# Kernel tuning notes

Hardware: AMD Instinct MI355X
Metric: run time of the kernel (lower is better)

The kernel has to match this reference:

```python
import jax, jax.numpy as jnp
import numpy as np

MARGIN = 0.2
ALPHA = 2.0
BETA = 1.5
ANGLE_THRESHOLD = 30.0
EPS_PD = 1e-6   # F.pairwise_distance eps
EPS_CS = 1e-8   # F.cosine_similarity eps
NEG_INF = -1e30
POS_INF = 1e30


def setup_inputs() -> dict:
    key = jax.random.key(0)
    k1, k2, k3 = jax.random.split(key, 3)
    B, F, A = 4096, 512, 3
    features = jax.random.normal(k1, (B, F), dtype=jnp.float32)
    labels = jax.random.randint(k2, (B,), 0, 256)
    angles = jax.random.uniform(k3, (B, A), dtype=jnp.float32) * 90.0  # degrees
    features_orig = jax.random.normal(jax.random.fold_in(key, 7), (B, F), dtype=jnp.float32)
    return {"features": features, "labels": labels, "angles": angles, "features_orig": features_orig}


def _cosine_sim_matrix(f):
    norms = jnp.linalg.norm(f, axis=1)
    denom = jnp.maximum(norms[:, None] * norms[None, :], EPS_CS)
    return (f @ f.T) / denom


def _forward(features, labels, angles, features_orig):
    B = features.shape[0]
    idx = jnp.arange(B)
    # pairwise angle distances [B,B] (torch.cdist p=2)
    adist = jnp.sqrt(jnp.sum((angles[:, None, :] - angles[None, :, :]) ** 2, axis=-1))
    same = labels[:, None] == labels[None, :]
    same = same & ~jnp.eye(B, dtype=bool)          # exclude self
    diff = labels[:, None] != labels[None, :]
    has_pos = same.any(axis=1)
    has_neg = diff.any(axis=1)
    valid = has_pos & has_neg
    # hardest positive: same label, largest angle difference
    pos_idx = jnp.argmax(jnp.where(same, adist, NEG_INF), axis=1)
    # hardest negative: among diff-label within angle threshold, most similar feature;
    # else diff-label with smallest angle difference
    sim = _cosine_sim_matrix(features)
    similar = diff & (adist < ANGLE_THRESHOLD)
    sim_any = similar.any(axis=1)
    neg_idx_hard = jnp.argmax(jnp.where(similar, sim, NEG_INF), axis=1)
    neg_idx_far = jnp.argmin(jnp.where(diff, adist, POS_INF), axis=1)
    neg_idx = jnp.where(sim_any, neg_idx_hard, neg_idx_far)
    # triplet distances (F.pairwise_distance adds eps to the diff)
    a = features
    p = features[pos_idx]
    n = features[neg_idx]
    pos_d = jnp.linalg.norm(a - p + EPS_PD, axis=1)
    neg_d = jnp.linalg.norm(a - n + EPS_PD, axis=1)
    # angle-based weights (non-differentiable, matches .item() in torch)
    pa = adist[idx, pos_idx]
    na = adist[idx, neg_idx]
    w = jnp.where(pa > 45.0, ALPHA, 1.0) * jnp.where(na < 15.0, BETA, 1.0)
    basic = jax.nn.relu(pos_d - neg_d + MARGIN)
    vmask = valid.astype(features.dtype)
    cnt = jnp.maximum(vmask.sum(), 1.0)
    triplet_loss = jnp.sum(w * basic * vmask) / cnt
    # reconstruction term
    num = jnp.sum(features * features_orig, axis=1)
    den = jnp.maximum(jnp.linalg.norm(features, axis=1) * jnp.linalg.norm(features_orig, axis=1), EPS_CS)
    recon = 1.0 - jnp.mean(num / den)
    return triplet_loss + 0.1 * recon


def reference(features, labels, angles, features_orig):
    return _forward(features, labels, angles, features_orig)
```

## Files before the change

### kernel.cpp

```cpp
#include <hip/hip_runtime.h>
#include <math.h>

#define BN 4096
#define FD 512
#define TT 128
#define BK 64
#define NJT (BN / TT)
#define NPAIR (NJT * (NJT + 1) / 2)
#define NBLK NPAIR
#define NPC 128
#define NJR 32
#define JR (BN / NJR)
#define NABLK (NJR * (BN / 256))

typedef __attribute__((ext_vector_type(8))) __bf16 bf16x8;
typedef __attribute__((ext_vector_type(4))) float floatx4;
typedef unsigned long long u64;

__device__ __forceinline__ float wred_sum(float v) {
#pragma unroll
  for (int m = 1; m < 64; m <<= 1) v += __shfl_xor(v, m, 64);
  return v;
}

__device__ __forceinline__ float dot4(float4 a, float4 b) {
  return a.x * b.x + a.y * b.y + a.z * b.z + a.w * b.w;
}

__device__ __forceinline__ unsigned short f2bf(float x) {
  unsigned u = __float_as_uint(x);
  u += 0x7fffu + ((u >> 16) & 1u);
  return (unsigned short)(u >> 16);
}

__device__ __forceinline__ void load16(const void* g, void* l) {
  __builtin_amdgcn_global_load_lds(
      (const __attribute__((address_space(1))) unsigned int*)g,
      (__attribute__((address_space(3))) unsigned int*)l, 16, 0, 0);
}

__device__ __forceinline__ unsigned ford(float v) {
  unsigned u = __float_as_uint(v);
  return u ^ (((unsigned)((int)u >> 31)) | 0x80000000u);
}

template <int N>
__device__ __forceinline__ int rori(int x) {
  return __builtin_amdgcn_update_dpp(0, x, 0x120 | N, 0xf, 0xf, true);
}
template <int N>
__device__ __forceinline__ u64 ror16_u64(u64 k) {
  unsigned lo = (unsigned)rori<N>((int)(unsigned)k);
  unsigned hi = (unsigned)rori<N>((int)(unsigned)(k >> 32));
  return ((u64)hi << 32) | lo;
}
__device__ __forceinline__ u64 red16_max_u64(u64 k) {
  u64 o;
  o = ror16_u64<1>(k); k = o > k ? o : k;
  o = ror16_u64<2>(k); k = o > k ? o : k;
  o = ror16_u64<4>(k); k = o > k ? o : k;
  o = ror16_u64<8>(k); k = o > k ? o : k;
  return k;
}

__device__ __forceinline__ u64 sx64(u64 v, int m) {
  unsigned lo = (unsigned)__shfl_xor((int)(unsigned)v, m, 64);
  unsigned hi = (unsigned)__shfl_xor((int)(unsigned)(v >> 32), m, 64);
  return ((u64)hi << 32) | lo;
}

__device__ __forceinline__ u64 umax64(u64 a, u64 b) { return a > b ? a : b; }

__global__ __launch_bounds__(256) void k_prep(const float* __restrict__ f,
                                              const float* __restrict__ fo,
                                              const float* __restrict__ angles,
                                              const int* __restrict__ labels,
                                              unsigned short* __restrict__ gb,
                                              float* __restrict__ rowr,
                                              float4* __restrict__ apk) {
  const int i = blockIdx.x * 4 + (threadIdx.x >> 6);
  const int lane = threadIdx.x & 63;
  const int t = blockIdx.x * 256 + threadIdx.x;
  if (t < BN) {
    float4 q;
    q.x = angles[t * 3 + 0];
    q.y = angles[t * 3 + 1];
    q.z = angles[t * 3 + 2];
    q.w = __uint_as_float((unsigned)labels[t]);
    apk[t] = q;
  }
  const float4* fr = (const float4*)(f + (size_t)i * FD);
  const float4* orr = (const float4*)(fo + (size_t)i * FD);
  float4 x0 = fr[lane], x1 = fr[lane + 64];
  float4 y0 = orr[lane], y1 = orr[lane + 64];
  float sff = dot4(x0, x0) + dot4(x1, x1);
  float sfo = dot4(x0, y0) + dot4(x1, y1);
  float soo = dot4(y0, y0) + dot4(y1, y1);
  sff = wred_sum(sff);
  sfo = wred_sum(sfo);
  soo = wred_sum(soo);
  float nf = sqrtf(sff);
  float inv = 1.0f / nf;
  ushort4* gr = (ushort4*)(gb + (size_t)i * FD);
  ushort4 s0, s1;
  s0.x = f2bf(x0.x * inv); s0.y = f2bf(x0.y * inv);
  s0.z = f2bf(x0.z * inv); s0.w = f2bf(x0.w * inv);
  s1.x = f2bf(x1.x * inv); s1.y = f2bf(x1.y * inv);
  s1.z = f2bf(x1.z * inv); s1.w = f2bf(x1.w * inv);
  gr[lane] = s0;
  gr[lane + 64] = s1;
  if (lane == 0) {
    rowr[i] = sfo / fmaxf(nf * sqrtf(soo), 1e-8f);
  }
}

__global__ __launch_bounds__(256, 4) void k_sim(const unsigned short* __restrict__ gb,
                                                const float4* __restrict__ apk,
                                                u64* __restrict__ pkey,
                                                u64* __restrict__ pangP,
                                                u64* __restrict__ pangN) {
  __shared__ __align__(16) unsigned short As[TT * BK];
  __shared__ __align__(16) unsigned short Bs[TT * BK];
  const int tid = threadIdx.x;

  if (blockIdx.x >= NBLK) {
    const int q = blockIdx.x - NBLK;
    const int jr = q & (NJR - 1);
    const int ib = q >> 5;
    const int i = ib * 256 + tid;
    float4* aj = (float4*)As;
    if (tid < JR) aj[tid] = apk[jr * JR + tid];
    __syncthreads();
    float4 me = apk[i];
    const unsigned lib = __float_as_uint(me.w);
    const int j0 = jr * JR;
    u64 keyP = 0, keyNc = 0;
#pragma unroll 4
    for (int jj = 0; jj < JR; jj++) {
      float4 aw = aj[jj];
      int j = j0 + jj;
      float d0 = me.x - aw.x;
      float d1 = me.y - aw.y;
      float d2 = me.z - aw.z;
      float dd = d0 * d0 + d1 * d1 + d2 * d2;
      u64 ddh = (u64)__float_as_uint(dd) << 32;
      bool same = (__float_as_uint(aw.w) == lib);
      u64 kp = ddh | (unsigned)(~j);
      if (same && j != i && kp > keyP) keyP = kp;
      u64 kn = ~(ddh | (unsigned)j);
      if (!same && kn > keyNc) keyNc = kn;
    }
    pangP[(size_t)jr * BN + i] = keyP;
    pangN[(size_t)jr * BN + i] = keyNc;
    return;
  }

  int a = 0, rem = blockIdx.x;
#pragma unroll 1
  while (rem >= NJT - a) { rem -= NJT - a; a++; }
  const int b = a + rem;
  const int i0 = a * TT;
  const int j0 = b * TT;

  const int w = tid >> 6;
  const int lane = tid & 63;
  const int wr = w >> 1;
  const int wc = w & 1;

  floatx4 acc[4][4];
#pragma unroll
  for (int u = 0; u < 4; u++)
#pragma unroll
    for (int v = 0; v < 4; v++) acc[u][v] = (floatx4){0.f, 0.f, 0.f, 0.f};

  const int rp = tid >> 3;
  const int q8 = ((tid & 7) ^ (rp & 7)) * 8;
  const unsigned short* gA[4];
  const unsigned short* gB[4];
  unsigned short* lA[4];
  unsigned short* lB[4];
#pragma unroll
  for (int c = 0; c < 4; c++) {
    gA[c] = gb + (size_t)(i0 + rp + 32 * c) * FD + q8;
    lA[c] = As + (tid + 256 * c) * 8;
    gB[c] = gb + (size_t)(j0 + rp + 32 * c) * FD + q8;
    lB[c] = Bs + (tid + 256 * c) * 8;
  }

  const int m = lane & 15;
  const int arow = wr * 64 + m;
  const int brow = wc * 64 + m;
  const int g4 = lane >> 4;
  const int l7 = lane & 7;
  const int koff0 = (g4 ^ l7) * 8;
  const int koff1 = ((4 + g4) ^ l7) * 8;

  for (int kc = 0; kc < FD; kc += BK) {
#pragma unroll
    for (int c = 0; c < 4; c++) load16(gA[c] + kc, lA[c]);
#pragma unroll
    for (int c = 0; c < 4; c++) load16(gB[c] + kc, lB[c]);
    __syncthreads();
    {
      bf16x8 af[4], bf[4];
#pragma unroll
      for (int u = 0; u < 4; u++)
        af[u] = *(const bf16x8*)(As + (arow + u * 16) * BK + koff0);
#pragma unroll
      for (int v = 0; v < 4; v++)
        bf[v] = *(const bf16x8*)(Bs + (brow + v * 16) * BK + koff0);
#pragma unroll
      for (int u = 0; u < 4; u++)
#pragma unroll
        for (int v = 0; v < 4; v++)
          acc[u][v] = __builtin_amdgcn_mfma_f32_16x16x32_bf16(af[u], bf[v], acc[u][v], 0, 0, 0);
#pragma unroll
      for (int u = 0; u < 4; u++)
        af[u] = *(const bf16x8*)(As + (arow + u * 16) * BK + koff1);
#pragma unroll
      for (int v = 0; v < 4; v++)
        bf[v] = *(const bf16x8*)(Bs + (brow + v * 16) * BK + koff1);
#pragma unroll
      for (int u = 0; u < 4; u++)
#pragma unroll
        for (int v = 0; v < 4; v++)
          acc[u][v] = __builtin_amdgcn_mfma_f32_16x16x32_bf16(af[u], bf[v], acc[u][v], 0, 0, 0);
    }
    __syncthreads();
  }

  const int quad = lane >> 4;
  const int cx = lane & 15;
  int jc[4];
  unsigned ljb[4];
  float jx[4], jy[4], jz[4];
#pragma unroll
  for (int v = 0; v < 4; v++) {
    jc[v] = j0 + wc * 64 + v * 16 + cx;
    float4 qj = apk[jc[v]];
    jx[v] = qj.x;
    jy[v] = qj.y;
    jz[v] = qj.z;
    ljb[v] = __float_as_uint(qj.w);
  }
  const size_t rbase = (size_t)(64 + 2 * b + wc) * BN;
  u64 ckey[4] = {0, 0, 0, 0};
#pragma unroll
  for (int u = 0; u < 4; u++) {
#pragma unroll
    for (int reg = 0; reg < 4; reg++) {
      int i = i0 + wr * 64 + u * 16 + quad * 4 + reg;
      float4 qi = apk[i];
      unsigned lib = __float_as_uint(qi.w);
      u64 rkey = 0;
      unsigned ni = (unsigned)(~i);
#pragma unroll
      for (int v = 0; v < 4; v++) {
        float d0 = qi.x - jx[v];
        float d1 = qi.y - jy[v];
        float d2 = qi.z - jz[v];
        float dd = d0 * d0 + d1 * d1 + d2 * d2;
        bool ok = (lib != ljb[v]) && (dd < 900.0f);
        u64 vh = (u64)ford(acc[u][v][reg]) << 32;
        u64 candR = vh | (unsigned)(~jc[v]);
        if (ok && candR > rkey) rkey = candR;
        u64 candC = vh | ni;
        if (ok && candC > ckey[v]) ckey[v] = candC;
      }
      rkey = red16_max_u64(rkey);
      if (cx == 0) pkey[rbase + i] = rkey;
    }
  }
  if (a != b) {
    const size_t cbase = (size_t)(4 * a + w) * BN;
#pragma unroll
    for (int v = 0; v < 4; v++) {
      u64 k = ckey[v];
      u64 o = sx64(k, 16); if (o > k) k = o;
      o = sx64(k, 32); if (o > k) k = o;
      if (quad == 0) pkey[cbase + jc[v]] = k;
    }
  }
}

__global__ __launch_bounds__(256) void k_final(const float* __restrict__ f,
                                               const float4* __restrict__ apk,
                                               const u64* __restrict__ pkey,
                                               const u64* __restrict__ pangP,
                                               const u64* __restrict__ pangN,
                                               float* __restrict__ rowc,
                                               float* __restrict__ rowv) {
  const int i = blockIdx.x * 4 + (threadIdx.x >> 6);
  const int lane = threadIdx.x & 63;
  const int t = i >> 7;
  const int p = (i >> 6) & 1;

  u64 s0 = ((lane < 4 * t) && ((lane & 1) == p)) ? pkey[(size_t)lane * BN + i] : 0;
  u64 s1 = (lane >= 2 * t) ? pkey[(size_t)(64 + lane) * BN + i] : 0;
  u64 keyS = umax64(s0, s1);
  u64 keyP = (lane < NJR) ? pangP[(size_t)lane * BN + i] : 0;
  u64 keyNc = (lane >= NJR) ? pangN[(size_t)(lane - NJR) * BN + i] : 0;
#pragma unroll
  for (int off = 1; off < 64; off <<= 1) {
    u64 o = sx64(keyS, off); if (o > keyS) keyS = o;
    o = sx64(keyP, off); if (o > keyP) keyP = o;
    o = sx64(keyNc, off); if (o > keyNc) keyNc = o;
  }
  bool hp = keyP != 0;
  bool hn = keyNc != 0;
  if (!(hp && hn)) {
    if (lane == 0) { rowc[i] = 0.0f; rowv[i] = 0.0f; }
    return;
  }
  bool sim_any = keyS != 0;
  int pos = (int)(~(unsigned)keyP);
  u64 keyN = ~keyNc;
  int neg = sim_any ? (int)(~(unsigned)keyS) : (int)(unsigned)keyN;

  const float4* fa = (const float4*)(f + (size_t)i * FD);
  const float4* fp = (const float4*)(f + (size_t)pos * FD);
  const float4* fn = (const float4*)(f + (size_t)neg * FD);
  float sp = 0.0f, sn = 0.0f;
#pragma unroll
  for (int t2 = 0; t2 < 2; t2++) {
    float4 xa = fa[lane + t2 * 64];
    float4 xp = fp[lane + t2 * 64];
    float4 xn = fn[lane + t2 * 64];
    float dp;
    dp = xa.x - xp.x + 1e-6f; sp += dp * dp;
    dp = xa.y - xp.y + 1e-6f; sp += dp * dp;
    dp = xa.z - xp.z + 1e-6f; sp += dp * dp;
    dp = xa.w - xp.w + 1e-6f; sp += dp * dp;
    dp = xa.x - xn.x + 1e-6f; sn += dp * dp;
    dp = xa.y - xn.y + 1e-6f; sn += dp * dp;
    dp = xa.z - xn.z + 1e-6f; sn += dp * dp;
    dp = xa.w - xn.w + 1e-6f; sn += dp * dp;
  }
  sp = wred_sum(sp);
  sn = wred_sum(sn);

  if (lane == 0) {
    float4 qi = apk[i];
    float4 qn = apk[neg];
    float pos_d = sqrtf(sp);
    float neg_d = sqrtf(sn);
    float pa = sqrtf(__uint_as_float((unsigned)(keyP >> 32)));
    float n0 = qi.x - qn.x;
    float n1 = qi.y - qn.y;
    float n2 = qi.z - qn.z;
    float na = sqrtf(n0 * n0 + n1 * n1 + n2 * n2);
    float w = (pa > 45.0f ? 2.0f : 1.0f) * (na < 15.0f ? 1.5f : 1.0f);
    float basic = fmaxf(pos_d - neg_d + 0.2f, 0.0f);
    rowc[i] = w * basic;
    rowv[i] = 1.0f;
  }
}

__global__ __launch_bounds__(1024) void k_out(const float* __restrict__ rowc,
                                              const float* __restrict__ rowv,
                                              const float* __restrict__ rowr,
                                              float* __restrict__ out) {
  __shared__ float sc[16], sv[16], sr[16];
  const int t = threadIdx.x;
  float c = 0.0f, v = 0.0f, r = 0.0f;
  for (int i = t; i < BN; i += 1024) {
    c += rowc[i];
    v += rowv[i];
    r += rowr[i];
  }
  c = wred_sum(c);
  v = wred_sum(v);
  r = wred_sum(r);
  const int wid = t >> 6;
  if ((t & 63) == 0) { sc[wid] = c; sv[wid] = v; sr[wid] = r; }
  __syncthreads();
  if (t == 0) {
    float C = 0.0f, V = 0.0f, R = 0.0f;
#pragma unroll
    for (int k = 0; k < 16; k++) { C += sc[k]; V += sv[k]; R += sr[k]; }
    float tri = C / fmaxf(V, 1.0f);
    float recon = 1.0f - R / (float)BN;
    out[0] = tri + 0.1f * recon;
  }
}

extern "C" void kernel_launch(void* const* d_in, const int* in_sizes, int n_in,
                              void* d_out, int out_size, void* d_ws, size_t ws_size,
                              hipStream_t stream) {
  const float* feat = (const float*)d_in[0];
  const int* labels = (const int*)d_in[1];
  const float* angles = (const float*)d_in[2];
  const float* forig = (const float*)d_in[3];
  float* out = (float*)d_out;

  char* ws = (char*)d_ws;
  unsigned short* gb = (unsigned short*)ws;
  size_t off = (size_t)BN * FD * sizeof(unsigned short);
  u64* pkey = (u64*)(ws + off);      off += (size_t)NPC * BN * 8;
  u64* pangP = (u64*)(ws + off);     off += (size_t)NJR * BN * 8;
  u64* pangN = (u64*)(ws + off);     off += (size_t)NJR * BN * 8;
  float4* apk = (float4*)(ws + off); off += (size_t)BN * 16;
  float* rowc = (float*)(ws + off);  off += (size_t)BN * 4;
  float* rowv = (float*)(ws + off);  off += (size_t)BN * 4;
  float* rowr = (float*)(ws + off);  off += (size_t)BN * 4;

  k_prep<<<BN / 4, 256, 0, stream>>>(feat, forig, angles, labels, gb, rowr, apk);
  k_sim<<<NBLK + NABLK, 256, 0, stream>>>(gb, apk, pkey, pangP, pangN);
  k_final<<<BN / 4, 256, 0, stream>>>(feat, apk, pkey, pangP, pangN, rowc, rowv);
  k_out<<<1, 1024, 0, stream>>>(rowc, rowv, rowr, out);
}
```

Measured before the change: 112.7 us.

## Double-buffer LDS tiles in similarity GEMM and skip B load on diagonal

```diff
diff --git a/kernel.cpp b/kernel.cpp
--- a/kernel.cpp
+++ b/kernel.cpp
@@ -5,6 +5,8 @@
 #define FD 512
 #define TT 128
 #define BK 64
+#define NK (FD / BK)
+#define TB (TT * BK)
 #define NJT (BN / TT)
 #define NPAIR (NJT * (NJT + 1) / 2)
 #define NBLK NPAIR
@@ -114,13 +116,13 @@
   }
 }
 
-__global__ __launch_bounds__(256, 4) void k_sim(const unsigned short* __restrict__ gb,
+__global__ __launch_bounds__(256, 2) void k_sim(const unsigned short* __restrict__ gb,
                                                 const float4* __restrict__ apk,
                                                 u64* __restrict__ pkey,
                                                 u64* __restrict__ pangP,
                                                 u64* __restrict__ pangN) {
-  __shared__ __align__(16) unsigned short As[TT * BK];
-  __shared__ __align__(16) unsigned short Bs[TT * BK];
+  __shared__ __align__(16) unsigned short As[2 * TB];
+  __shared__ __align__(16) unsigned short Bs[2 * TB];
   const int tid = threadIdx.x;
 
   if (blockIdx.x >= NBLK) {
@@ -161,6 +163,7 @@
   const int b = a + rem;
   const int i0 = a * TT;
   const int j0 = b * TT;
+  const bool diag = (a == b);
 
   const int w = tid >> 6;
   const int lane = tid & 63;
@@ -195,20 +198,37 @@
   const int koff0 = (g4 ^ l7) * 8;
   const int koff1 = ((4 + g4) ^ l7) * 8;
 
-  for (int kc = 0; kc < FD; kc += BK) {
-#pragma unroll
-    for (int c = 0; c < 4; c++) load16(gA[c] + kc, lA[c]);
-#pragma unroll
-    for (int c = 0; c < 4; c++) load16(gB[c] + kc, lB[c]);
-    __syncthreads();
+#pragma unroll
+  for (int c = 0; c < 4; c++) load16(gA[c], lA[c]);
+  if (!diag) {
+#pragma unroll
+    for (int c = 0; c < 4; c++) load16(gB[c], lB[c]);
+  }
+  asm volatile("s_waitcnt vmcnt(0)" ::: "memory");
+  __syncthreads();
+
+  for (int t = 0; t < NK; t++) {
+    const int cur = (t & 1) * TB;
+    if (t + 1 < NK) {
+      const int nxt = ((t + 1) & 1) * TB;
+      const int kc = (t + 1) * BK;
+#pragma unroll
+      for (int c = 0; c < 4; c++) load16(gA[c] + kc, lA[c] + nxt);
+      if (!diag) {
+#pragma unroll
+        for (int c = 0; c < 4; c++) load16(gB[c] + kc, lB[c] + nxt);
+      }
+    }
+    const unsigned short* Ab = As + cur;
+    const unsigned short* Bb = (diag ? As : Bs) + cur;
     {
       bf16x8 af[4], bf[4];
 #pragma unroll
       for (int u = 0; u < 4; u++)
-        af[u] = *(const bf16x8*)(As + (arow + u * 16) * BK + koff0);
+        af[u] = *(const bf16x8*)(Ab + (arow + u * 16) * BK + koff0);
 #pragma unroll
       for (int v = 0; v < 4; v++)
-        bf[v] = *(const bf16x8*)(Bs + (brow + v * 16) * BK + koff0);
+        bf[v] = *(const bf16x8*)(Bb + (brow + v * 16) * BK + koff0);
 #pragma unroll
       for (int u = 0; u < 4; u++)
 #pragma unroll
@@ -216,16 +236,17 @@
           acc[u][v] = __builtin_amdgcn_mfma_f32_16x16x32_bf16(af[u], bf[v], acc[u][v], 0, 0, 0);
 #pragma unroll
       for (int u = 0; u < 4; u++)
-        af[u] = *(const bf16x8*)(As + (arow + u * 16) * BK + koff1);
+        af[u] = *(const bf16x8*)(Ab + (arow + u * 16) * BK + koff1);
 #pragma unroll
       for (int v = 0; v < 4; v++)
-        bf[v] = *(const bf16x8*)(Bs + (brow + v * 16) * BK + koff1);
+        bf[v] = *(const bf16x8*)(Bb + (brow + v * 16) * BK + koff1);
 #pragma unroll
       for (int u = 0; u < 4; u++)
 #pragma unroll
         for (int v = 0; v < 4; v++)
           acc[u][v] = __builtin_amdgcn_mfma_f32_16x16x32_bf16(af[u], bf[v], acc[u][v], 0, 0, 0);
     }
+    asm volatile("s_waitcnt vmcnt(0)" ::: "memory");
     __syncthreads();
   }
 
```

Result: no change. 114.2 us (+1.3%).
